# Kernel optimization log

Hardware: AMD Instinct MI355X
Metric: run time of the kernel (lower is better)

## Reference

```python
import jax, jax.numpy as jnp
import numpy as np

L, D, C, H = 2, 2, 256, 128  # layers, directions, channels, hidden (= C//2, bidirectional)
B, T = 32, 1024


def setup_inputs() -> dict:
    key = jax.random.key(0)
    ks = jax.random.split(key, 5)
    k = 1.0 / np.sqrt(H)  # PyTorch LSTM init scale
    u = lambda kk, shape: jax.random.uniform(kk, shape, jnp.float32, -k, k)
    return {
        "x": jax.random.normal(ks[0], (B, C, T), jnp.float32),
        "W_ih": u(ks[1], (L, D, 4 * H, C)),  # layer1 input is concat(fwd,bwd) = C wide too
        "W_hh": u(ks[2], (L, D, 4 * H, H)),
        "b_ih": u(ks[3], (L, D, 4 * H)),
        "b_hh": u(ks[4], (L, D, 4 * H)),
    }


def _lstm_dir(xs, Wih, Whh, bih, bhh, reverse):
    # xs: [T, B, C_in] time-major; returns hidden states [T, B, H]
    Tn, Bn, _ = xs.shape
    Hh = Whh.shape[1]
    # precompute input contribution to all gates for every timestep (one big GEMM)
    gx = jnp.einsum('tbc,gc->tbg', xs, Wih) + bih + bhh  # [T, B, 4H]

    def step(carry, g):
        h, c = carry
        g = g + h @ Whh.T  # [B, 4H]
        i, f, gg, o = jnp.split(g, 4, axis=-1)  # PyTorch gate order: i, f, g, o
        c = jax.nn.sigmoid(f) * c + jax.nn.sigmoid(i) * jnp.tanh(gg)
        h = jax.nn.sigmoid(o) * jnp.tanh(c)
        return (h, c), h

    init = (jnp.zeros((Bn, Hh), xs.dtype), jnp.zeros((Bn, Hh), xs.dtype))
    _, hs = jax.lax.scan(step, init, gx, reverse=reverse)
    return hs


def reference(x, W_ih, W_hh, b_ih, b_hh):
    # x: [B, C, T] -> time-major [T, B, C] (matches x.transpose(1,2) with batch_first)
    h = jnp.transpose(x, (2, 0, 1))
    for l in range(L):
        fwd = _lstm_dir(h, W_ih[l, 0], W_hh[l, 0], b_ih[l, 0], b_hh[l, 0], False)
        bwd = _lstm_dir(h, W_ih[l, 1], W_hh[l, 1], b_ih[l, 1], b_hh[l, 1], True)
        h = jnp.concatenate([fwd, bwd], axis=-1)  # [T, B, 2H] = [T, B, C]
    # back to [B, C, T] (matches out.transpose(1,2))
    return jnp.transpose(h, (1, 2, 0))
```

## Files before the change

kernel.cpp:

```cpp
#include <hip/hip_runtime.h>
#include <cstdint>
#include <cstddef>

static constexpr int TT = 1024;
static constexpr int BB = 32;
static constexpr int CC = 256;
static constexpr int HH = 128;
static constexpr int GG = 512;
static constexpr int MM = TT * BB;

typedef float f32x2 __attribute__((ext_vector_type(2)));

__device__ __forceinline__ float fsig(float x) { return 1.f / (1.f + __expf(-x)); }
__device__ __forceinline__ float ftanh(float x) {
  float e = __expf(2.f * x);
  return 1.f - 2.f / (e + 1.f);
}

__global__ __launch_bounds__(256) void k_transpose_in(const float* __restrict__ x,
                                                      float* __restrict__ xs) {
  __shared__ float tile[32][33];
  const int t0 = blockIdx.x * 32, c0 = blockIdx.y * 32, b = blockIdx.z;
  const int tx = threadIdx.x, ty = threadIdx.y;
#pragma unroll
  for (int i = 0; i < 4; i++) {
    const int cc = ty + i * 8;
    tile[cc][tx] = x[((size_t)b * CC + (c0 + cc)) * TT + t0 + tx];
  }
  __syncthreads();
#pragma unroll
  for (int i = 0; i < 4; i++) {
    const int tt = ty + i * 8;
    xs[((size_t)(t0 + tt) * BB + b) * CC + c0 + tx] = tile[tx][tt];
  }
}

__global__ __launch_bounds__(256) void k_transpose_out(const float* __restrict__ h2,
                                                       float* __restrict__ out) {
  __shared__ float tile[32][33];
  const int t0 = blockIdx.x * 32, c0 = blockIdx.y * 32, b = blockIdx.z;
  const int tx = threadIdx.x, ty = threadIdx.y;
#pragma unroll
  for (int i = 0; i < 4; i++) {
    const int tt = ty + i * 8;
    tile[tt][tx] = h2[((size_t)(t0 + tt) * BB + b) * CC + c0 + tx];
  }
  __syncthreads();
#pragma unroll
  for (int i = 0; i < 4; i++) {
    const int cc = ty + i * 8;
    out[((size_t)b * CC + (c0 + cc)) * TT + t0 + tx] = tile[tx][cc];
  }
}

__global__ __launch_bounds__(256) void k_gemm_ih(const float* __restrict__ X,
                                                 const float* __restrict__ W,
                                                 const float* __restrict__ bih,
                                                 const float* __restrict__ bhh,
                                                 float* __restrict__ gx, int M) {
  const int d = blockIdx.z;
  const int row0 = blockIdx.y * 128;
  const int col0 = blockIdx.x * 64;
  const float* Wd = W + (size_t)d * GG * CC;
  __shared__ float As[16][132];
  __shared__ float Ws[16][68];
  const int tid = threadIdx.x;
  const int tm = tid >> 4;
  const int tn = tid & 15;
  const int lr = tid >> 2;
  const int lk = (tid & 3) * 4;

  float acc[8][4] = {};
  for (int k0 = 0; k0 < CC; k0 += 16) {
    const float4 a0 = *(const float4*)&X[(size_t)(row0 + lr) * CC + k0 + lk];
    const float4 a1 = *(const float4*)&X[(size_t)(row0 + 64 + lr) * CC + k0 + lk];
    const float4 wv = *(const float4*)&Wd[(size_t)(col0 + lr) * CC + k0 + lk];
    __syncthreads();
    As[lk + 0][lr] = a0.x; As[lk + 1][lr] = a0.y; As[lk + 2][lr] = a0.z; As[lk + 3][lr] = a0.w;
    As[lk + 0][64 + lr] = a1.x; As[lk + 1][64 + lr] = a1.y; As[lk + 2][64 + lr] = a1.z; As[lk + 3][64 + lr] = a1.w;
    Ws[lk + 0][lr] = wv.x; Ws[lk + 1][lr] = wv.y; Ws[lk + 2][lr] = wv.z; Ws[lk + 3][lr] = wv.w;
    __syncthreads();
#pragma unroll
    for (int kk = 0; kk < 16; kk++) {
      const float4 av0 = *(const float4*)&As[kk][tm * 8];
      const float4 av1 = *(const float4*)&As[kk][tm * 8 + 4];
      const float4 bv = *(const float4*)&Ws[kk][tn * 4];
      const float a[8] = {av0.x, av0.y, av0.z, av0.w, av1.x, av1.y, av1.z, av1.w};
      const float bb4[4] = {bv.x, bv.y, bv.z, bv.w};
#pragma unroll
      for (int i = 0; i < 8; i++)
#pragma unroll
        for (int j = 0; j < 4; j++) acc[i][j] = fmaf(a[i], bb4[j], acc[i][j]);
    }
  }
  float bias[4];
#pragma unroll
  for (int j = 0; j < 4; j++) {
    const int col = col0 + tn * 4 + j;
    bias[j] = bih[d * GG + col] + bhh[d * GG + col];
  }
#pragma unroll
  for (int i = 0; i < 8; i++) {
    const int row = row0 + tm * 8 + i;
    float4 o;
    o.x = acc[i][0] + bias[0];
    o.y = acc[i][1] + bias[1];
    o.z = acc[i][2] + bias[2];
    o.w = acc[i][3] + bias[3];
    *(float4*)&gx[((size_t)d * M + row) * GG + col0 + tn * 4] = o;
  }
}

__global__ __launch_bounds__(512, 1) void k_lstm_rec(const float* __restrict__ gx,
                                                     const float* __restrict__ Whh,
                                                     float* __restrict__ hout) {
  const int b = blockIdx.x & 31;
  const int d = blockIdx.x >> 5;
  const int tid = threadIdx.x;
  const int q = tid >> 7;
  const int j = tid & 127;
  __shared__ __align__(16) float h_s[HH];
  __shared__ __align__(16) float part[4][HH][4];

  f32x2 w2[4][16];
  {
    const float* base = Whh + (size_t)d * GG * HH;
#pragma unroll
    for (int gi = 0; gi < 4; gi++) {
      const float4* wrow = (const float4*)(base + (size_t)(gi * HH + j) * HH + q * 32);
#pragma unroll
      for (int k = 0; k < 8; k++) {
        const float4 t4 = wrow[k];
        w2[gi][2 * k]     = f32x2{t4.x, t4.y};
        w2[gi][2 * k + 1] = f32x2{t4.z, t4.w};
      }
    }
  }
#pragma unroll
  for (int gi = 0; gi < 4; gi++) {
    asm volatile("" : "+v"(w2[gi][0]), "+v"(w2[gi][1]), "+v"(w2[gi][2]), "+v"(w2[gi][3]),
                      "+v"(w2[gi][4]), "+v"(w2[gi][5]), "+v"(w2[gi][6]), "+v"(w2[gi][7]));
    asm volatile("" : "+v"(w2[gi][8]), "+v"(w2[gi][9]), "+v"(w2[gi][10]), "+v"(w2[gi][11]),
                      "+v"(w2[gi][12]), "+v"(w2[gi][13]), "+v"(w2[gi][14]), "+v"(w2[gi][15]));
  }

  if (tid < HH) h_s[tid] = 0.f;
  float c = 0.f;

  const float* gxb = gx + ((size_t)d * TT * BB + b) * (size_t)GG;
  const size_t stride = (size_t)BB * GG;
  int t = d ? (TT - 1) : 0;
  const int tdir = d ? -1 : 1;
  const bool is_act = (tid < HH);

  float gxc0 = 0.f, gxc1 = 0.f, gxc2 = 0.f, gxc3 = 0.f;
  if (is_act) {
    const float* g0 = gxb + (size_t)t * stride + j;
    gxc0 = g0[0]; gxc1 = g0[HH]; gxc2 = g0[2 * HH]; gxc3 = g0[3 * HH];
  }
  __syncthreads();

  for (int s = 0; s < TT; s++) {
    float gxn0 = 0.f, gxn1 = 0.f, gxn2 = 0.f, gxn3 = 0.f;
    if (is_act && s + 1 < TT) {
      const float* g0 = gxb + (size_t)(t + tdir) * stride + j;
      gxn0 = g0[0]; gxn1 = g0[HH]; gxn2 = g0[2 * HH]; gxn3 = g0[3 * HH];
    }

    f32x2 hp[16];
    {
      const float4* hq = (const float4*)(h_s + q * 32);
#pragma unroll
      for (int k = 0; k < 8; k++) {
        const float4 hv = hq[k];
        hp[2 * k]     = f32x2{hv.x, hv.y};
        hp[2 * k + 1] = f32x2{hv.z, hv.w};
      }
    }

    f32x2 a0a = {0.f, 0.f}, a0b = {0.f, 0.f}, a1a = {0.f, 0.f}, a1b = {0.f, 0.f};
    f32x2 a2a = {0.f, 0.f}, a2b = {0.f, 0.f}, a3a = {0.f, 0.f}, a3b = {0.f, 0.f};
#pragma unroll
    for (int k = 0; k < 8; k++) {
      asm("v_pk_fma_f32 %0, %8, %16, %0\n\t"
          "v_pk_fma_f32 %1, %9, %17, %1\n\t"
          "v_pk_fma_f32 %2, %10, %16, %2\n\t"
          "v_pk_fma_f32 %3, %11, %17, %3\n\t"
          "v_pk_fma_f32 %4, %12, %16, %4\n\t"
          "v_pk_fma_f32 %5, %13, %17, %5\n\t"
          "v_pk_fma_f32 %6, %14, %16, %6\n\t"
          "v_pk_fma_f32 %7, %15, %17, %7"
          : "+v"(a0a), "+v"(a0b), "+v"(a1a), "+v"(a1b),
            "+v"(a2a), "+v"(a2b), "+v"(a3a), "+v"(a3b)
          : "v"(w2[0][2 * k]), "v"(w2[0][2 * k + 1]),
            "v"(w2[1][2 * k]), "v"(w2[1][2 * k + 1]),
            "v"(w2[2][2 * k]), "v"(w2[2][2 * k + 1]),
            "v"(w2[3][2 * k]), "v"(w2[3][2 * k + 1]),
            "v"(hp[2 * k]), "v"(hp[2 * k + 1]));
    }
    const float A0 = (a0a.x + a0a.y) + (a0b.x + a0b.y);
    const float A1 = (a1a.x + a1a.y) + (a1b.x + a1b.y);
    const float A2 = (a2a.x + a2a.y) + (a2b.x + a2b.y);
    const float A3 = (a3a.x + a3a.y) + (a3b.x + a3b.y);
    *(float4*)&part[q][j][0] = make_float4(A0, A1, A2, A3);
    __syncthreads();

    if (is_act) {
      const float4 p0 = *(const float4*)&part[0][j][0];
      const float4 p1 = *(const float4*)&part[1][j][0];
      const float4 p2 = *(const float4*)&part[2][j][0];
      const float4 p3 = *(const float4*)&part[3][j][0];
      const float i_g = fsig(p0.x + p1.x + p2.x + p3.x + gxc0);
      const float f_g = fsig(p0.y + p1.y + p2.y + p3.y + gxc1);
      const float g_g = ftanh(p0.z + p1.z + p2.z + p3.z + gxc2);
      const float o_g = fsig(p0.w + p1.w + p2.w + p3.w + gxc3);
      c = f_g * c + i_g * g_g;
      const float h = o_g * ftanh(c);
      h_s[j] = h;
      hout[((size_t)t * BB + b) * CC + d * HH + j] = h;
    }
    __syncthreads();
    gxc0 = gxn0; gxc1 = gxn1; gxc2 = gxn2; gxc3 = gxn3;
    t += tdir;
  }
}

extern "C" void kernel_launch(void* const* d_in, const int* in_sizes, int n_in,
                              void* d_out, int out_size, void* d_ws, size_t ws_size,
                              hipStream_t stream) {
  const float* x    = (const float*)d_in[0];
  const float* W_ih = (const float*)d_in[1];
  const float* W_hh = (const float*)d_in[2];
  const float* b_ih = (const float*)d_in[3];
  const float* b_hh = (const float*)d_in[4];
  float* out = (float*)d_out;

  if (ws_size < (size_t)160 * 1024 * 1024) return;

  char* ws = (char*)d_ws;
  float* xs = (float*)ws;
  float* gxbuf = (float*)(ws + (size_t)32 * 1024 * 1024);
  float* h1 = out;
  float* h2 = xs;

  const dim3 tb(32, 8);
  const dim3 tg(TT / 32, CC / 32, BB);

  k_transpose_in<<<tg, tb, 0, stream>>>(x, xs);
  k_gemm_ih<<<dim3(GG / 64, MM / 128, 2), 256, 0, stream>>>(xs, W_ih, b_ih, b_hh, gxbuf, MM);
  k_lstm_rec<<<64, 512, 0, stream>>>(gxbuf, W_hh, h1);
  k_gemm_ih<<<dim3(GG / 64, MM / 128, 2), 256, 0, stream>>>(h1, W_ih + 2 * GG * CC,
                                                            b_ih + 2 * GG, b_hh + 2 * GG, gxbuf, MM);
  k_lstm_rec<<<64, 512, 0, stream>>>(gxbuf, W_hh + 2 * GG * HH, h2);
  k_transpose_out<<<tg, tb, 0, stream>>>(h2, out);
}
```

Measured before the change: 2.206 ms.

## Use split-bf16 MFMA GEMM for input projections with bf16 hi/lo activations

Replaces the FP32 SIMT input-projection GEMM with an MFMA bf16 GEMM. Each fp32 operand is split into hi and lo bf16 parts and three products are summed, so accuracy stays close to fp32. The input transpose and the layer-1 recurrence now write hi/lo bf16 copies directly. Weights are split on the fly inside the GEMM, with swizzled LDS tiles. The recurrent kernel's hand-written packed-FMA asm is replaced by vector-typed C code, which the compiler may or may not schedule as well. The recurrence dominates runtime, so the GEMM speedup covers only a small share of the total.

```diff
diff --git a/kernel.cpp b/kernel.cpp
--- a/kernel.cpp
+++ b/kernel.cpp
@@ -10,15 +10,28 @@
 static constexpr int MM = TT * BB;
 
 typedef float f32x2 __attribute__((ext_vector_type(2)));
+typedef float f32x4v __attribute__((ext_vector_type(4)));
+typedef short bf16x8 __attribute__((ext_vector_type(8)));
 
 __device__ __forceinline__ float fsig(float x) { return 1.f / (1.f + __expf(-x)); }
 __device__ __forceinline__ float ftanh(float x) {
   float e = __expf(2.f * x);
   return 1.f - 2.f / (e + 1.f);
 }
-
-__global__ __launch_bounds__(256) void k_transpose_in(const float* __restrict__ x,
-                                                      float* __restrict__ xs) {
+__device__ __forceinline__ ushort bf16_rn(float x) {
+  union { float f; uint u; } v; v.f = x;
+  const uint r = v.u + 0x7fffu + ((v.u >> 16) & 1u);
+  return (ushort)(r >> 16);
+}
+__device__ __forceinline__ float bf16_to_f(ushort h) {
+  union { uint u; float f; } v; v.u = ((uint)h) << 16;
+  return v.f;
+}
+__device__ __forceinline__ uint pack2(ushort a, ushort b) { return (uint)a | ((uint)b << 16); }
+
+__global__ __launch_bounds__(256) void k_transpose_cvt_in(const float* __restrict__ x,
+                                                          ushort* __restrict__ xhi,
+                                                          ushort* __restrict__ xlo) {
   __shared__ float tile[32][33];
   const int t0 = blockIdx.x * 32, c0 = blockIdx.y * 32, b = blockIdx.z;
   const int tx = threadIdx.x, ty = threadIdx.y;
@@ -31,7 +44,11 @@
 #pragma unroll
   for (int i = 0; i < 4; i++) {
     const int tt = ty + i * 8;
-    xs[((size_t)(t0 + tt) * BB + b) * CC + c0 + tx] = tile[tx][tt];
+    const float v = tile[tx][tt];
+    const ushort hi = bf16_rn(v);
+    const size_t idx = ((size_t)(t0 + tt) * BB + b) * CC + c0 + tx;
+    xhi[idx] = hi;
+    xlo[idx] = bf16_rn(v - bf16_to_f(hi));
   }
 }
 
@@ -53,67 +70,109 @@
   }
 }
 
-__global__ __launch_bounds__(256) void k_gemm_ih(const float* __restrict__ X,
-                                                 const float* __restrict__ W,
-                                                 const float* __restrict__ bih,
-                                                 const float* __restrict__ bhh,
-                                                 float* __restrict__ gx, int M) {
+__global__ __launch_bounds__(256) void k_gemm_mfma(const ushort* __restrict__ Ahi,
+                                                   const ushort* __restrict__ Alo,
+                                                   const float* __restrict__ W,
+                                                   const float* __restrict__ bih,
+                                                   const float* __restrict__ bhh,
+                                                   float* __restrict__ gx) {
   const int d = blockIdx.z;
-  const int row0 = blockIdx.y * 128;
-  const int col0 = blockIdx.x * 64;
+  const int g0 = blockIdx.x * 64;
+  const int m0 = blockIdx.y * 128;
   const float* Wd = W + (size_t)d * GG * CC;
-  __shared__ float As[16][132];
-  __shared__ float Ws[16][68];
+
+  __shared__ ushort Ah[128][64];
+  __shared__ ushort Al[128][64];
+  __shared__ ushort Bh[64][64];
+  __shared__ ushort Bl[64][64];
+
   const int tid = threadIdx.x;
-  const int tm = tid >> 4;
-  const int tn = tid & 15;
-  const int lr = tid >> 2;
-  const int lk = (tid & 3) * 4;
-
-  float acc[8][4] = {};
-  for (int k0 = 0; k0 < CC; k0 += 16) {
-    const float4 a0 = *(const float4*)&X[(size_t)(row0 + lr) * CC + k0 + lk];
-    const float4 a1 = *(const float4*)&X[(size_t)(row0 + 64 + lr) * CC + k0 + lk];
-    const float4 wv = *(const float4*)&Wd[(size_t)(col0 + lr) * CC + k0 + lk];
+  const int lane = tid & 63;
+  const int wid = tid >> 6;
+  const int wm = (wid >> 1) * 64;
+  const int wg = (wid & 1) * 32;
+
+  f32x4v acc[4][2] = {};
+
+  for (int k0 = 0; k0 < CC; k0 += 64) {
     __syncthreads();
-    As[lk + 0][lr] = a0.x; As[lk + 1][lr] = a0.y; As[lk + 2][lr] = a0.z; As[lk + 3][lr] = a0.w;
-    As[lk + 0][64 + lr] = a1.x; As[lk + 1][64 + lr] = a1.y; As[lk + 2][64 + lr] = a1.z; As[lk + 3][64 + lr] = a1.w;
-    Ws[lk + 0][lr] = wv.x; Ws[lk + 1][lr] = wv.y; Ws[lk + 2][lr] = wv.z; Ws[lk + 3][lr] = wv.w;
+#pragma unroll
+    for (int c = 0; c < 4; c++) {
+      const int f8 = c * 256 + tid;
+      const int r = f8 >> 3;
+      const int kb = f8 & 7;
+      const int sw = (kb ^ (r & 7)) << 3;
+      const uint4 vh = *(const uint4*)&Ahi[(size_t)(m0 + r) * CC + k0 + kb * 8];
+      const uint4 vl = *(const uint4*)&Alo[(size_t)(m0 + r) * CC + k0 + kb * 8];
+      *(uint4*)&Ah[r][sw] = vh;
+      *(uint4*)&Al[r][sw] = vl;
+    }
+#pragma unroll
+    for (int c = 0; c < 4; c++) {
+      const int f4 = c * 256 + tid;
+      const int g = f4 >> 4;
+      const int k4 = f4 & 15;
+      const float4 wv = *(const float4*)&Wd[(size_t)(g0 + g) * CC + k0 + k4 * 4];
+      ushort h0 = bf16_rn(wv.x), h1 = bf16_rn(wv.y), h2 = bf16_rn(wv.z), h3 = bf16_rn(wv.w);
+      ushort l0 = bf16_rn(wv.x - bf16_to_f(h0)), l1 = bf16_rn(wv.y - bf16_to_f(h1));
+      ushort l2 = bf16_rn(wv.z - bf16_to_f(h2)), l3 = bf16_rn(wv.w - bf16_to_f(h3));
+      const int off = (((k4 >> 1) ^ (g & 7)) << 3) | ((k4 & 1) * 4);
+      uint2 ph; ph.x = pack2(h0, h1); ph.y = pack2(h2, h3);
+      uint2 pl; pl.x = pack2(l0, l1); pl.y = pack2(l2, l3);
+      *(uint2*)&Bh[g][off] = ph;
+      *(uint2*)&Bl[g][off] = pl;
+    }
     __syncthreads();
 #pragma unroll
-    for (int kk = 0; kk < 16; kk++) {
-      const float4 av0 = *(const float4*)&As[kk][tm * 8];
-      const float4 av1 = *(const float4*)&As[kk][tm * 8 + 4];
-      const float4 bv = *(const float4*)&Ws[kk][tn * 4];
-      const float a[8] = {av0.x, av0.y, av0.z, av0.w, av1.x, av1.y, av1.z, av1.w};
-      const float bb4[4] = {bv.x, bv.y, bv.z, bv.w};
-#pragma unroll
-      for (int i = 0; i < 8; i++)
-#pragma unroll
-        for (int j = 0; j < 4; j++) acc[i][j] = fmaf(a[i], bb4[j], acc[i][j]);
-    }
-  }
-  float bias[4];
-#pragma unroll
-  for (int j = 0; j < 4; j++) {
-    const int col = col0 + tn * 4 + j;
-    bias[j] = bih[d * GG + col] + bhh[d * GG + col];
-  }
-#pragma unroll
-  for (int i = 0; i < 8; i++) {
-    const int row = row0 + tm * 8 + i;
-    float4 o;
-    o.x = acc[i][0] + bias[0];
-    o.y = acc[i][1] + bias[1];
-    o.z = acc[i][2] + bias[2];
-    o.w = acc[i][3] + bias[3];
-    *(float4*)&gx[((size_t)d * M + row) * GG + col0 + tn * 4] = o;
+    for (int h = 0; h < 2; h++) {
+      const int kb = h * 4 + (lane >> 4);
+      bf16x8 afh[4], afl[4], bfh[2], bfl[2];
+#pragma unroll
+      for (int i = 0; i < 4; i++) {
+        const int row = wm + i * 16 + (lane & 15);
+        const int sw = (kb ^ (row & 7)) << 3;
+        afh[i] = *(const bf16x8*)&Ah[row][sw];
+        afl[i] = *(const bf16x8*)&Al[row][sw];
+      }
+#pragma unroll
+      for (int j = 0; j < 2; j++) {
+        const int gr = wg + j * 16 + (lane & 15);
+        const int sw = (kb ^ (gr & 7)) << 3;
+        bfh[j] = *(const bf16x8*)&Bh[gr][sw];
+        bfl[j] = *(const bf16x8*)&Bl[gr][sw];
+      }
+#pragma unroll
+      for (int i = 0; i < 4; i++)
+#pragma unroll
+        for (int j = 0; j < 2; j++) {
+          acc[i][j] = __builtin_amdgcn_mfma_f32_16x16x32_bf16(afh[i], bfh[j], acc[i][j], 0, 0, 0);
+          acc[i][j] = __builtin_amdgcn_mfma_f32_16x16x32_bf16(afh[i], bfl[j], acc[i][j], 0, 0, 0);
+          acc[i][j] = __builtin_amdgcn_mfma_f32_16x16x32_bf16(afl[i], bfh[j], acc[i][j], 0, 0, 0);
+        }
+    }
+  }
+  const int col = lane & 15;
+  const int rbase = (lane >> 4) * 4;
+#pragma unroll
+  for (int j = 0; j < 2; j++) {
+    const int g = g0 + wg + j * 16 + col;
+    const float bias = bih[d * GG + g] + bhh[d * GG + g];
+#pragma unroll
+    for (int i = 0; i < 4; i++) {
+      const int mrow = m0 + wm + i * 16 + rbase;
+#pragma unroll
+      for (int rr = 0; rr < 4; rr++)
+        gx[((size_t)d * MM + mrow + rr) * GG + g] = acc[i][j][rr] + bias;
+    }
   }
 }
 
 __global__ __launch_bounds__(512, 1) void k_lstm_rec(const float* __restrict__ gx,
                                                      const float* __restrict__ Whh,
-                                                     float* __restrict__ hout) {
+                                                     float* __restrict__ hf32,
+                                                     ushort* __restrict__ hhi,
+                                                     ushort* __restrict__ hlo,
+                                                     int store_bf16) {
   const int b = blockIdx.x & 31;
   const int d = blockIdx.x >> 5;
   const int tid = threadIdx.x;
@@ -131,18 +190,16 @@
 #pragma unroll
       for (int k = 0; k < 8; k++) {
         const float4 t4 = wrow[k];
-        w2[gi][2 * k]     = f32x2{t4.x, t4.y};
+        w2[gi][2 * k] = f32x2{t4.x, t4.y};
         w2[gi][2 * k + 1] = f32x2{t4.z, t4.w};
       }
     }
   }
 #pragma unroll
-  for (int gi = 0; gi < 4; gi++) {
-    asm volatile("" : "+v"(w2[gi][0]), "+v"(w2[gi][1]), "+v"(w2[gi][2]), "+v"(w2[gi][3]),
-                      "+v"(w2[gi][4]), "+v"(w2[gi][5]), "+v"(w2[gi][6]), "+v"(w2[gi][7]));
-    asm volatile("" : "+v"(w2[gi][8]), "+v"(w2[gi][9]), "+v"(w2[gi][10]), "+v"(w2[gi][11]),
-                      "+v"(w2[gi][12]), "+v"(w2[gi][13]), "+v"(w2[gi][14]), "+v"(w2[gi][15]));
-  }
+  for (int gi = 0; gi < 4; gi++)
+#pragma unroll
+    for (int k = 0; k < 16; k++)
+      asm volatile("" : "+v"(w2[gi][k]));
 
   if (tid < HH) h_s[tid] = 0.f;
   float c = 0.f;
@@ -173,35 +230,24 @@
 #pragma unroll
       for (int k = 0; k < 8; k++) {
         const float4 hv = hq[k];
-        hp[2 * k]     = f32x2{hv.x, hv.y};
+        hp[2 * k] = f32x2{hv.x, hv.y};
         hp[2 * k + 1] = f32x2{hv.z, hv.w};
       }
     }
 
-    f32x2 a0a = {0.f, 0.f}, a0b = {0.f, 0.f}, a1a = {0.f, 0.f}, a1b = {0.f, 0.f};
-    f32x2 a2a = {0.f, 0.f}, a2b = {0.f, 0.f}, a3a = {0.f, 0.f}, a3b = {0.f, 0.f};
+    f32x2 aA0 = {0.f, 0.f}, aA1 = {0.f, 0.f}, aA2 = {0.f, 0.f}, aA3 = {0.f, 0.f};
+    f32x2 aB0 = {0.f, 0.f}, aB1 = {0.f, 0.f}, aB2 = {0.f, 0.f}, aB3 = {0.f, 0.f};
 #pragma unroll
     for (int k = 0; k < 8; k++) {
-      asm("v_pk_fma_f32 %0, %8, %16, %0\n\t"
-          "v_pk_fma_f32 %1, %9, %17, %1\n\t"
-          "v_pk_fma_f32 %2, %10, %16, %2\n\t"
-          "v_pk_fma_f32 %3, %11, %17, %3\n\t"
-          "v_pk_fma_f32 %4, %12, %16, %4\n\t"
-          "v_pk_fma_f32 %5, %13, %17, %5\n\t"
-          "v_pk_fma_f32 %6, %14, %16, %6\n\t"
-          "v_pk_fma_f32 %7, %15, %17, %7"
-          : "+v"(a0a), "+v"(a0b), "+v"(a1a), "+v"(a1b),
-            "+v"(a2a), "+v"(a2b), "+v"(a3a), "+v"(a3b)
-          : "v"(w2[0][2 * k]), "v"(w2[0][2 * k + 1]),
-            "v"(w2[1][2 * k]), "v"(w2[1][2 * k + 1]),
-            "v"(w2[2][2 * k]), "v"(w2[2][2 * k + 1]),
-            "v"(w2[3][2 * k]), "v"(w2[3][2 * k + 1]),
-            "v"(hp[2 * k]), "v"(hp[2 * k + 1]));
-    }
-    const float A0 = (a0a.x + a0a.y) + (a0b.x + a0b.y);
-    const float A1 = (a1a.x + a1a.y) + (a1b.x + a1b.y);
-    const float A2 = (a2a.x + a2a.y) + (a2b.x + a2b.y);
-    const float A3 = (a3a.x + a3a.y) + (a3b.x + a3b.y);
+      aA0 = w2[0][2 * k] * hp[2 * k] + aA0;  aB0 = w2[0][2 * k + 1] * hp[2 * k + 1] + aB0;
+      aA1 = w2[1][2 * k] * hp[2 * k] + aA1;  aB1 = w2[1][2 * k + 1] * hp[2 * k + 1] + aB1;
+      aA2 = w2[2][2 * k] * hp[2 * k] + aA2;  aB2 = w2[2][2 * k + 1] * hp[2 * k + 1] + aB2;
+      aA3 = w2[3][2 * k] * hp[2 * k] + aA3;  aB3 = w2[3][2 * k + 1] * hp[2 * k + 1] + aB3;
+    }
+    const float A0 = (aA0.x + aA0.y) + (aB0.x + aB0.y);
+    const float A1 = (aA1.x + aA1.y) + (aB1.x + aB1.y);
+    const float A2 = (aA2.x + aA2.y) + (aB2.x + aB2.y);
+    const float A3 = (aA3.x + aA3.y) + (aB3.x + aB3.y);
     *(float4*)&part[q][j][0] = make_float4(A0, A1, A2, A3);
     __syncthreads();
 
@@ -217,7 +263,14 @@
       c = f_g * c + i_g * g_g;
       const float h = o_g * ftanh(c);
       h_s[j] = h;
-      hout[((size_t)t * BB + b) * CC + d * HH + j] = h;
+      const size_t idx = ((size_t)t * BB + b) * CC + d * HH + j;
+      if (store_bf16) {
+        const ushort hi = bf16_rn(h);
+        hhi[idx] = hi;
+        hlo[idx] = bf16_rn(h - bf16_to_f(hi));
+      } else {
+        hf32[idx] = h;
+      }
     }
     __syncthreads();
     gxc0 = gxn0; gxc1 = gxn1; gxc2 = gxn2; gxc3 = gxn3;
@@ -238,19 +291,20 @@
   if (ws_size < (size_t)160 * 1024 * 1024) return;
 
   char* ws = (char*)d_ws;
-  float* xs = (float*)ws;
-  float* gxbuf = (float*)(ws + (size_t)32 * 1024 * 1024);
-  float* h1 = out;
-  float* h2 = xs;
+  ushort* abf_hi = (ushort*)ws;
+  ushort* abf_lo = (ushort*)(ws + (size_t)16 * 1024 * 1024);
+  float*  h2     = (float*)ws;
+  float*  gxbuf  = (float*)(ws + (size_t)32 * 1024 * 1024);
 
   const dim3 tb(32, 8);
   const dim3 tg(TT / 32, CC / 32, BB);
-
-  k_transpose_in<<<tg, tb, 0, stream>>>(x, xs);
-  k_gemm_ih<<<dim3(GG / 64, MM / 128, 2), 256, 0, stream>>>(xs, W_ih, b_ih, b_hh, gxbuf, MM);
-  k_lstm_rec<<<64, 512, 0, stream>>>(gxbuf, W_hh, h1);
-  k_gemm_ih<<<dim3(GG / 64, MM / 128, 2), 256, 0, stream>>>(h1, W_ih + 2 * GG * CC,
-                                                            b_ih + 2 * GG, b_hh + 2 * GG, gxbuf, MM);
-  k_lstm_rec<<<64, 512, 0, stream>>>(gxbuf, W_hh + 2 * GG * HH, h2);
+  const dim3 gemm_grid(GG / 64, MM / 128, 2);
+
+  k_transpose_cvt_in<<<tg, tb, 0, stream>>>(x, abf_hi, abf_lo);
+  k_gemm_mfma<<<gemm_grid, 256, 0, stream>>>(abf_hi, abf_lo, W_ih, b_ih, b_hh, gxbuf);
+  k_lstm_rec<<<64, 512, 0, stream>>>(gxbuf, W_hh, nullptr, abf_hi, abf_lo, 1);
+  k_gemm_mfma<<<gemm_grid, 256, 0, stream>>>(abf_hi, abf_lo, W_ih + 2 * GG * CC,
+                                             b_ih + 2 * GG, b_hh + 2 * GG, gxbuf);
+  k_lstm_rec<<<64, 512, 0, stream>>>(gxbuf, W_hh + 2 * GG * HH, h2, nullptr, nullptr, 0);
   k_transpose_out<<<tg, tb, 0, stream>>>(h2, out);
 }
```

Result: faster. 1.819 ms (-17.6%).
